# Performance work log

Hardware: AMD Instinct MI355X
Metric: run time of the kernel (lower is better)

Reference implementation:

```python
import jax, jax.numpy as jnp
import numpy as np

B, C, H, D, W = 1, 32, 32, 32, 32   # batch, channels, 3D grid
M1 = M2 = M3 = 16                   # fourier modes kept per dim
KS = 3                              # spatial attention kernel size
MEM = 5                             # memory slots
EPS = 1e-5
N = H * D * W


def _gelu(x):
    return jax.nn.gelu(x, approximate=False)  # torch exact GELU


def _gn(x):
    # GroupNorm(1, C) without affine: normalize over (C,H,D,W) per sample
    mu = jnp.mean(x, axis=(1, 2, 3, 4), keepdims=True)
    var = jnp.var(x, axis=(1, 2, 3, 4), keepdims=True)
    return (x - mu) * jax.lax.rsqrt(var + EPS)


def _spectral_conv(x, wr, wi):
    # classic 3D FNO spectral conv: keep low modes (4 corner blocks in dims H,D; low block in rfft dim W)
    xf = jnp.fft.rfftn(x, axes=(2, 3, 4))                 # (B,C,H,D,W//2+1) complex64
    w = wr + 1j * wi                                      # (4,Cin,Cout,M1,M2,M3)
    of = jnp.zeros((x.shape[0], C, H, D, W // 2 + 1), xf.dtype)
    corners = [(slice(0, M1), slice(0, M2)), (slice(H - M1, H), slice(0, M2)),
               (slice(0, M1), slice(D - M2, D)), (slice(H - M1, H), slice(D - M2, D))]
    for i, (s1, s2) in enumerate(corners):
        of = of.at[:, :, s1, s2, :M3].set(
            jnp.einsum('bixyz,ioxyz->boxyz', xf[:, :, s1, s2, :M3], w[i]))
    return jnp.fft.irfftn(of, s=(H, D, W), axes=(2, 3, 4))


def _forward(x, t, prev_memory, w_spec_r, w_spec_i, norm1_g, norm1_b,
             mlp_w1, mlp_b1, mlp_w2, mlp_b2, tin_gw, tin_gb, tin_bw, tin_bb,
             q_w, q_b, k_w, k_b, v_w, v_b, mem_key, mem_value,
             gate_w, gate_b, gru_wih, gru_whh, gru_bih, gru_bhh):
    skip1 = x
    skip2 = _gelu(x)
    # spectral conv -> GroupNorm(affine) + residual -> gelu
    h = _spectral_conv(x, w_spec_r, w_spec_i)
    h = _gelu(_gn(h) * norm1_g[None, :, None, None, None]
              + norm1_b[None, :, None, None, None] + skip1)
    # pointwise Conv1d MLP over channels
    hf = h.reshape(B, C, N)
    u = _gelu(jnp.einsum('oc,bcn->bon', mlp_w1, hf) + mlp_b1[None, :, None])
    hf = jnp.einsum('oc,bcn->bon', mlp_w2, u) + mlp_b2[None, :, None]
    h = hf.reshape(B, C, H, D, W)
    # time-conditioned instance norm: gamma/beta from 1x1 conv over t (B,C)
    gamma = (jnp.einsum('oc,bc->bo', tin_gw, t) + tin_gb)[:, :, None, None, None]
    beta = (jnp.einsum('oc,bc->bo', tin_bw, t) + tin_bb)[:, :, None, None, None]
    h = gamma * _gn(h) + beta
    # ---- spatial attention with memory ----
    pad = KS // 2
    xp = jnp.pad(h, ((0, 0), (0, 0), (pad, pad), (pad, pad), (pad, pad)))
    # 3D unfold: (B,C,27,N) patches via 27 shifted views
    patches = jnp.stack([xp[:, :, i:i + H, j:j + D, l:l + W]
                         for i in range(KS) for j in range(KS) for l in range(KS)],
                        axis=2).reshape(B, C, KS ** 3, N)
    hf = h.reshape(B, C, N)
    q = jnp.einsum('oc,bcn->bon', q_w, hf) + q_b[None, :, None]              # (B,C,N)
    k_sp = jnp.einsum('oc,bcmn->bomn', k_w, patches) + k_b[None, :, None, None]
    v_sp = jnp.einsum('oc,bcmn->bomn', v_w, patches) + v_b[None, :, None, None]
    mem_k = jnp.broadcast_to(mem_key[None, :, :, None], (B, C, MEM, N))
    mem_v = jnp.broadcast_to(mem_value[None, :, :, None], (B, C, MEM, N))
    k = jnp.concatenate([mem_k, k_sp], axis=2)                               # (B,C,32,N)
    v = jnp.concatenate([mem_v, v_sp], axis=2)
    attn = jax.nn.softmax(q[:, :, None, :] * k / jnp.sqrt(jnp.float32(C)), axis=2)
    out = jnp.sum(attn * v, axis=2)                                          # (B,C,N)
    cat = jnp.concatenate([hf, out], axis=1)                                 # (B,2C,N)
    gate = jax.nn.sigmoid(jnp.einsum('oc,bcn->bon', gate_w, cat) + gate_b[None, :, None])
    out = gate * out + (1.0 - gate) * hf
    out = out.reshape(B, C, H, D, W)
    # GRUCell memory update from spatially pooled features
    m_in = jnp.mean(out, axis=(2, 3, 4))                                     # (B,C)
    gi = m_in @ gru_wih.T + gru_bih
    gh = prev_memory @ gru_whh.T + gru_bhh
    ir, iz, inn = jnp.split(gi, 3, axis=1)
    hr, hz, hn = jnp.split(gh, 3, axis=1)
    r = jax.nn.sigmoid(ir + hr)
    z = jax.nn.sigmoid(iz + hz)
    n = jnp.tanh(inn + r * hn)
    new_memory = (1.0 - z) * n + z * prev_memory                             # (B,C)
    return out + skip2, new_memory


def setup_inputs():
    key = jax.random.key(0)
    ks = jax.random.split(key, 20)
    def rn(k, shape, s):
        return jax.random.normal(k, shape, jnp.float32) * s
    spec_scale = 1.0 / (C * C)
    return dict(
        x=jax.random.normal(ks[0], (B, C, H, D, W), jnp.float32),
        t=jax.random.normal(ks[1], (B, C), jnp.float32),
        prev_memory=jnp.zeros((B, C), jnp.float32),
        w_spec_r=rn(ks[2], (4, C, C, M1, M2, M3), spec_scale),
        w_spec_i=rn(ks[3], (4, C, C, M1, M2, M3), spec_scale),
        norm1_g=jnp.ones((C,), jnp.float32),
        norm1_b=jnp.zeros((C,), jnp.float32),
        mlp_w1=rn(ks[4], (C // 2, C), 0.1), mlp_b1=jnp.zeros((C // 2,), jnp.float32),
        mlp_w2=rn(ks[5], (C, C // 2), 0.1), mlp_b2=jnp.zeros((C,), jnp.float32),
        tin_gw=rn(ks[6], (C, C), 0.1), tin_gb=jnp.ones((C,), jnp.float32),
        tin_bw=rn(ks[7], (C, C), 0.1), tin_bb=jnp.zeros((C,), jnp.float32),
        q_w=rn(ks[8], (C, C), 0.1), q_b=jnp.zeros((C,), jnp.float32),
        k_w=rn(ks[9], (C, C), 0.1), k_b=jnp.zeros((C,), jnp.float32),
        v_w=rn(ks[10], (C, C), 0.1), v_b=jnp.zeros((C,), jnp.float32),
        mem_key=jax.random.normal(ks[11], (C, MEM), jnp.float32),
        mem_value=jax.random.normal(ks[12], (C, MEM), jnp.float32),
        gate_w=rn(ks[13], (C, 2 * C), 0.1), gate_b=jnp.zeros((C,), jnp.float32),
        gru_wih=rn(ks[14], (3 * C, C), 0.1), gru_whh=rn(ks[15], (3 * C, C), 0.1),
        gru_bih=jnp.zeros((3 * C,), jnp.float32), gru_bhh=jnp.zeros((3 * C,), jnp.float32),
    )


def reference(x, t, prev_memory, w_spec_r, w_spec_i, norm1_g, norm1_b,
              mlp_w1, mlp_b1, mlp_w2, mlp_b2, tin_gw, tin_gb, tin_bw, tin_bb,
              q_w, q_b, k_w, k_b, v_w, v_b, mem_key, mem_value,
              gate_w, gate_b, gru_wih, gru_whh, gru_bih, gru_bhh):
    return _forward(x, t, prev_memory, w_spec_r, w_spec_i, norm1_g, norm1_b,
                    mlp_w1, mlp_b1, mlp_w2, mlp_b2, tin_gw, tin_gb, tin_bw, tin_bb,
                    q_w, q_b, k_w, k_b, v_w, v_b, mem_key, mem_value,
                    gate_w, gate_b, gru_wih, gru_whh, gru_bih, gru_bhh)
```

## Files before the change

### kernel.cpp

```cpp
#include <hip/hip_runtime.h>
#include <hip/hip_bf16.h>
#include <math.h>

#define NSP 32768
#define NZ 17

__device__ __forceinline__ float geluf(float x){
    return 0.5f * x * (1.0f + erff(x * 0.70710678118654752f));
}
__device__ __forceinline__ float sigmoidf_(float x){
    return 1.0f / (1.0f + __expf(-x));
}


__global__ void k_fwd(const float* __restrict__ x, float* __restrict__ Br, float* __restrict__ Bi){
    __shared__ float tile[32*33];
    __shared__ float ar[544], ai[544];
    __shared__ float ct[32], st[32];
    int b = blockIdx.x, t = threadIdx.x;
    if (t < 32){ float ang = 6.283185307179586477f * (float)t / 32.0f; ct[t] = cosf(ang); st[t] = sinf(ang); }
    const float* src = x + b * 1024;
    for (int j = t; j < 1024; j += 256) tile[(j & 31) * 33 + (j >> 5)] = src[j];
    __syncthreads();
    for (int idx = t; idx < 544; idx += 256){
        int d = idx / 17, z = idx - d * 17;
        float sr = 0.f, si = 0.f;
        #pragma unroll
        for (int w = 0; w < 32; ++w){
            int a = (z * w) & 31;
            float v = tile[w * 33 + d];
            sr += v * ct[a];
            si -= v * st[a];
        }
        ar[idx] = sr; ai[idx] = si;
    }
    __syncthreads();
    for (int idx = t; idx < 544; idx += 256){
        int kd = idx / 17, z = idx - kd * 17;
        float sr = 0.f, si = 0.f;
        #pragma unroll
        for (int d = 0; d < 32; ++d){
            int a = (kd * d) & 31;
            float c = ct[a], s = st[a];
            float vr = ar[d * 17 + z], vi = ai[d * 17 + z];
            sr += vr * c + vi * s;
            si += vi * c - vr * s;
        }
        Br[b * 544 + idx] = sr; Bi[b * 544 + idx] = si;
    }
}

__global__ void k_fft_h(const float* __restrict__ Br, const float* __restrict__ Bi,
                        float* __restrict__ Ar, float* __restrict__ Ai){
    __shared__ float ir[544], ii[544];
    __shared__ float ct[32], st[32];
    int b = blockIdx.x, t = threadIdx.x;
    int c = b >> 5, d = b & 31;
    if (t < 32){ float ang = 6.283185307179586477f * (float)t / 32.0f; ct[t] = cosf(ang); st[t] = sinf(ang); }
    for (int j = t; j < 544; j += 256){
        int h = j / 17, z = j - h * 17;
        int g = ((c * 32 + h) * 32 + d) * NZ + z;
        ir[j] = Br[g]; ii[j] = Bi[g];
    }
    __syncthreads();
    for (int idx = t; idx < 544; idx += 256){
        int kh = idx / 17, z = idx - kh * 17;
        float sr = 0.f, si = 0.f;
        #pragma unroll
        for (int h = 0; h < 32; ++h){
            int a = (kh * h) & 31;
            float c2 = ct[a], s2 = st[a];
            float vr = ir[h * 17 + z], vi = ii[h * 17 + z];
            sr += vr * c2 + vi * s2;
            si += vi * c2 - vr * s2;
        }
        int g = ((c * 32 + kh) * 32 + d) * NZ + z;
        Ar[g] = sr; Ai[g] = si;
    }
}

__global__ void k_modemul(const float* __restrict__ Xr, const float* __restrict__ Xi,
                          const float* __restrict__ Wr, const float* __restrict__ Wi,
                          float* __restrict__ Or, float* __restrict__ Oi){
    __shared__ float xr[32 * 64], xi[32 * 64];
    int b = blockIdx.x;
    int corner = b >> 6;
    int xm = (b >> 2) & 15;
    int ymg = b & 3;
    int xg = xm + ((corner & 1) << 4);
    int ybase = ymg * 4 + ((corner >> 1) << 4);
    int t = threadIdx.x;
    for (int idx = t; idx < 2048; idx += 1024){
        int i = idx >> 6, m = idx & 63;
        int y = ybase + (m >> 4), z = m & 15;
        int g = ((i * 32 + xg) * 32 + y) * NZ + z;
        xr[idx] = Xr[g]; xi[idx] = Xi[g];
    }
    if (t < 128){
        int o = t >> 2, y = ybase + (t & 3);
        int g = ((o * 32 + xg) * 32 + y) * NZ + 16;
        Or[g] = 0.f; Oi[g] = 0.f;
    }
    __syncthreads();
    int wv = t >> 6, lane = t & 63;
    int o0 = wv * 2, o1 = o0 + 1;
    float ar0 = 0.f, ai0 = 0.f, ar1 = 0.f, ai1 = 0.f;
    int wtail = xm * 256 + ymg * 64 + lane;
    for (int i = 0; i < 32; ++i){
        float vxr = xr[i * 64 + lane], vxi = xi[i * 64 + lane];
        long base = (long)((corner * 32 + i) * 32) * 4096 + wtail;
        float w0r = Wr[base + o0 * 4096], w0i = Wi[base + o0 * 4096];
        float w1r = Wr[base + o1 * 4096], w1i = Wi[base + o1 * 4096];
        ar0 += w0r * vxr - w0i * vxi;
        ai0 += w0r * vxi + w0i * vxr;
        ar1 += w1r * vxr - w1i * vxi;
        ai1 += w1r * vxi + w1i * vxr;
    }
    int y = ybase + (lane >> 4), z = lane & 15;
    int g0 = ((o0 * 32 + xg) * 32 + y) * NZ + z;
    int g1 = ((o1 * 32 + xg) * 32 + y) * NZ + z;
    Or[g0] = ar0; Oi[g0] = ai0;
    Or[g1] = ar1; Oi[g1] = ai1;
}

__global__ void k_ifft_h(const float* __restrict__ Br, const float* __restrict__ Bi,
                         float* __restrict__ Ar, float* __restrict__ Ai){
    __shared__ float ir[544], ii[544];
    __shared__ float ct[32], st[32];
    int b = blockIdx.x, t = threadIdx.x;
    int c = b >> 5, y = b & 31;
    if (t < 32){ float ang = 6.283185307179586477f * (float)t / 32.0f; ct[t] = cosf(ang); st[t] = sinf(ang); }
    for (int j = t; j < 544; j += 256){
        int xk = j / 17, z = j - xk * 17;
        int g = ((c * 32 + xk) * 32 + y) * NZ + z;
        ir[j] = Br[g]; ii[j] = Bi[g];
    }
    __syncthreads();
    for (int idx = t; idx < 544; idx += 256){
        int h = idx / 17, z = idx - h * 17;
        float sr = 0.f, si = 0.f;
        #pragma unroll
        for (int k = 0; k < 32; ++k){
            int a = (k * h) & 31;
            float c2 = ct[a], s2 = st[a];
            float vr = ir[k * 17 + z], vi = ii[k * 17 + z];
            sr += vr * c2 - vi * s2;
            si += vr * s2 + vi * c2;
        }
        int g = ((c * 32 + h) * 32 + y) * NZ + z;
        Ar[g] = sr; Ai[g] = si;
    }
}

__global__ void k_inv(const float* __restrict__ Ar, const float* __restrict__ Ai,
                      float* __restrict__ spec,
                      float* __restrict__ psum, float* __restrict__ psq){
    __shared__ float ir[544], ii[544];
    __shared__ float cr[544], ci[544];
    __shared__ float ct[32], st[32];
    __shared__ float ls[256], lq[256];
    int b = blockIdx.x, t = threadIdx.x;
    if (t < 32){ float ang = 6.283185307179586477f * (float)t / 32.0f; ct[t] = cosf(ang); st[t] = sinf(ang); }
    const float* pr = Ar + b * 544;
    const float* pi = Ai + b * 544;
    for (int j = t; j < 544; j += 256){ ir[j] = pr[j]; ii[j] = pi[j]; }
    __syncthreads();
    for (int idx = t; idx < 544; idx += 256){
        int d = idx / 17, z = idx - d * 17;
        float sr = 0.f, si = 0.f;
        #pragma unroll
        for (int k = 0; k < 32; ++k){
            int a = (k * d) & 31;
            float c2 = ct[a], s2 = st[a];
            float vr = ir[k * 17 + z], vi = ii[k * 17 + z];
            sr += vr * c2 - vi * s2;
            si += vr * s2 + vi * c2;
        }
        cr[idx] = sr; ci[idx] = si;
    }
    __syncthreads();
    const float inv = 1.0f / 32768.0f;
    float s_loc = 0.f, q_loc = 0.f;
    for (int idx = t; idx < 1024; idx += 256){
        int d = idx >> 5, w = idx & 31;
        float s = cr[d * 17 + 0] + ((w & 1) ? -cr[d * 17 + 16] : cr[d * 17 + 16]);
        #pragma unroll
        for (int z = 1; z < 16; ++z){
            int a = (z * w) & 31;
            s += 2.0f * (cr[d * 17 + z] * ct[a] - ci[d * 17 + z] * st[a]);
        }
        s *= inv;
        spec[b * 1024 + idx] = s;
        s_loc += s; q_loc += s * s;
    }
    ls[t] = s_loc; lq[t] = q_loc; __syncthreads();
    for (int off = 128; off > 0; off >>= 1){
        if (t < off){ ls[t] += ls[t + off]; lq[t] += lq[t + off]; }
        __syncthreads();
    }
    if (t == 0){ psum[b] = ls[0]; psq[b] = lq[0]; }
}


__global__ void k_finalize1(const float* __restrict__ psum, const float* __restrict__ psq,
                            int n, float* __restrict__ red){
    __shared__ float ls[256], lq[256];
    int t = threadIdx.x;
    float s = 0.f, q = 0.f;
    for (int j = t; j < n; j += 256){ s += psum[j]; q += psq[j]; }
    ls[t] = s; lq[t] = q; __syncthreads();
    for (int off = 128; off > 0; off >>= 1){
        if (t < off){ ls[t] += ls[t + off]; lq[t] += lq[t + off]; }
        __syncthreads();
    }
    if (t == 0){
        float mu = ls[0] * (1.0f / 1048576.0f);
        float var = lq[0] * (1.0f / 1048576.0f) - mu * mu;
        red[0] = mu; red[1] = rsqrtf(var + 1e-5f);
    }
}

__global__ void k_finalize2(const float* __restrict__ psum, const float* __restrict__ psq,
                            int n, const float* __restrict__ tin,
                            const float* __restrict__ tgw, const float* __restrict__ tgb,
                            const float* __restrict__ tbw, const float* __restrict__ tbb,
                            float* __restrict__ red){
    __shared__ float ls[256], lq[256];
    int t = threadIdx.x;
    float s = 0.f, q = 0.f;
    for (int j = t; j < n; j += 256){ s += psum[j]; q += psq[j]; }
    ls[t] = s; lq[t] = q; __syncthreads();
    for (int off = 128; off > 0; off >>= 1){
        if (t < off){ ls[t] += ls[t + off]; lq[t] += lq[t + off]; }
        __syncthreads();
    }
    if (t == 0){
        float mu = ls[0] * (1.0f / 1048576.0f);
        float var = lq[0] * (1.0f / 1048576.0f) - mu * mu;
        red[2] = mu; red[3] = rsqrtf(var + 1e-5f);
    }
    if (t < 64){
        int o = t & 31;
        const float* w = (t < 32) ? tgw : tbw;
        const float* bi = (t < 32) ? tgb : tbb;
        float a = bi[o];
        #pragma unroll
        for (int c = 0; c < 32; ++c) a += w[o * 32 + c] * tin[c];
        red[(t < 32 ? 16 : 48) + o] = a;
    }
}

__global__ void k_mlp(const float* __restrict__ spec, const float* __restrict__ x,
                      const float* __restrict__ n1g, const float* __restrict__ n1b,
                      const float* __restrict__ red,
                      const float* __restrict__ w1, const float* __restrict__ b1,
                      const float* __restrict__ w2, const float* __restrict__ b2,
                      float* __restrict__ h2,
                      float* __restrict__ psum, float* __restrict__ psq){
    __shared__ float W1[512], W2[512], B1[16], B2[32], GG[32], BB[32];
    __shared__ float ls[256], lq[256];
    int t = threadIdx.x;
    for (int j = t; j < 512; j += 256){ W1[j] = w1[j]; W2[j] = w2[j]; }
    if (t < 16) B1[t] = b1[t];
    if (t < 32){ B2[t] = b2[t]; GG[t] = n1g[t]; BB[t] = n1b[t]; }
    __syncthreads();
    float mu = red[0], rs = red[1];
    int n = blockIdx.x * 256 + t;
    float hv[32];
    #pragma unroll
    for (int c = 0; c < 32; ++c){
        float v = (spec[c * NSP + n] - mu) * rs * GG[c] + BB[c] + x[c * NSP + n];
        hv[c] = geluf(v);
    }
    float u[16];
    #pragma unroll
    for (int o = 0; o < 16; ++o){
        float a = B1[o];
        #pragma unroll
        for (int c = 0; c < 32; ++c) a += W1[o * 32 + c] * hv[c];
        u[o] = geluf(a);
    }
    float s_loc = 0.f, q_loc = 0.f;
    #pragma unroll
    for (int o = 0; o < 32; ++o){
        float a = B2[o];
        #pragma unroll
        for (int c = 0; c < 16; ++c) a += W2[o * 16 + c] * u[c];
        h2[o * NSP + n] = a;
        s_loc += a; q_loc += a * a;
    }
    ls[t] = s_loc; lq[t] = q_loc; __syncthreads();
    for (int off = 128; off > 0; off >>= 1){
        if (t < off){ ls[t] += ls[t + off]; lq[t] += lq[t + off]; }
        __syncthreads();
    }
    if (t == 0){ psum[blockIdx.x] = ls[0]; psq[blockIdx.x] = lq[0]; }
}

__global__ void k_qkv(const float* __restrict__ h2, const float* __restrict__ red,
                      const float* __restrict__ qw, const float* __restrict__ qb,
                      const float* __restrict__ kw, const float* __restrict__ vw,
                      float* __restrict__ h3, float* __restrict__ Q,
                      float* __restrict__ KH, float* __restrict__ VH){
    __shared__ float QW[1024], KW[1024], VW[1024], GA[32], BE[32], QB[32];
    int t = threadIdx.x;
    for (int j = t; j < 1024; j += 256){ QW[j] = qw[j]; KW[j] = kw[j]; VW[j] = vw[j]; }
    if (t < 32){ GA[t] = red[16 + t]; BE[t] = red[48 + t]; QB[t] = qb[t]; }
    __syncthreads();
    float mu = red[2], rs = red[3];
    int n = blockIdx.x * 256 + t;
    float hv[32];
    #pragma unroll
    for (int c = 0; c < 32; ++c){
        float v = GA[c] * ((h2[c * NSP + n] - mu) * rs) + BE[c];
        hv[c] = v;
        h3[c * NSP + n] = v;
    }
    #pragma unroll
    for (int o = 0; o < 32; ++o){
        float aq = QB[o], ak = 0.f, av = 0.f;
        #pragma unroll
        for (int c = 0; c < 32; ++c){
            float v = hv[c];
            aq += QW[o * 32 + c] * v;
            ak += KW[o * 32 + c] * v;
            av += VW[o * 32 + c] * v;
        }
        Q[o * NSP + n] = aq;
        KH[o * NSP + n] = ak;
        VH[o * NSP + n] = av;
    }
}

__global__ void k_attn(const float* __restrict__ Q, const float* __restrict__ KH,
                       const float* __restrict__ VH,
                       const float* __restrict__ kb, const float* __restrict__ vb,
                       const float* __restrict__ mk, const float* __restrict__ mv,
                       float* __restrict__ out0){
    __shared__ float KL[3][1024], VL[3][1024];
    int bid = blockIdx.x;
    int swz = (bid & 7) * 128 + (bid >> 3);
    int c = swz >> 5, h_ = swz & 31;
    int t = threadIdx.x;
    #pragma unroll
    for (int p = 0; p < 3; ++p){
        int hh = h_ - 1 + p;
        if ((unsigned)hh < 32u){
            const float* sk = KH + (c * 32 + hh) * 1024;
            const float* sv = VH + (c * 32 + hh) * 1024;
            for (int j = t; j < 1024; j += 256){ KL[p][j] = sk[j]; VL[p][j] = sv[j]; }
        }
    }
    float kbc = kb[c], vbc = vb[c];
    float mkv[5], mvv[5];
    #pragma unroll
    for (int j = 0; j < 5; ++j){ mkv[j] = mk[c * 5 + j]; mvv[j] = mv[c * 5 + j]; }
    float qv[4];
    #pragma unroll
    for (int i = 0; i < 4; ++i) qv[i] = Q[c * NSP + h_ * 1024 + i * 256 + t];
    __syncthreads();
    const float scale = 0.17677669529663688f;
    #pragma unroll
    for (int i = 0; i < 4; ++i){
        int nl = i * 256 + t;
        int d_ = nl >> 5, w_ = nl & 31;
        float q = qv[i];
        float s = 0.f, acc = 0.f;
        #pragma unroll
        for (int j = 0; j < 5; ++j){
            float e = __expf(q * mkv[j] * scale);
            s += e; acc += e * mvv[j];
        }
        int oob = 0;
        #pragma unroll
        for (int p = 0; p < 3; ++p){
            int hh = h_ - 1 + p;
            if ((unsigned)hh >= 32u){ oob += 9; continue; }
            #pragma unroll
            for (int dj = -1; dj <= 1; ++dj){
                int dd = d_ + dj;
                if ((unsigned)dd >= 32u){ oob += 3; continue; }
                int rb = dd * 32;
                #pragma unroll
                for (int dl = -1; dl <= 1; ++dl){
                    int ww = w_ + dl;
                    if ((unsigned)ww < 32u){
                        float k = kbc + KL[p][rb + ww];
                        float v = vbc + VL[p][rb + ww];
                        float e = __expf(q * k * scale);
                        s += e; acc += e * v;
                    } else oob++;
                }
            }
        }
        float eb = __expf(q * kbc * scale);
        s += (float)oob * eb; acc += (float)oob * eb * vbc;
        out0[c * NSP + h_ * 1024 + nl] = acc / s;
    }
}

__global__ void k_gate(const float* __restrict__ h3, const float* __restrict__ out0,
                       const float* __restrict__ x,
                       const float* __restrict__ gw, const float* __restrict__ gb,
                       float* __restrict__ outp, float* __restrict__ mpart){
    __shared__ float GW[2048];
    __shared__ float FT[32 * 264];
    __shared__ float PS[256];
    int t = threadIdx.x;
    for (int j = t; j < 2048; j += 256) GW[j] = gw[j];
    int n = blockIdx.x * 256 + t;
    float hv[32], ov[32];
    #pragma unroll
    for (int c = 0; c < 32; ++c){ hv[c] = h3[c * NSP + n]; ov[c] = out0[c * NSP + n]; }
    __syncthreads();
    #pragma unroll
    for (int c = 0; c < 32; ++c){
        float g = gb[c];
        #pragma unroll
        for (int cc = 0; cc < 32; ++cc){
            g += GW[c * 64 + cc] * hv[cc] + GW[c * 64 + 32 + cc] * ov[cc];
        }
        g = sigmoidf_(g);
        float fin = g * ov[c] + (1.0f - g) * hv[c];
        FT[c * 264 + t] = fin;
        outp[c * NSP + n] = fin + geluf(x[c * NSP + n]);
    }
    __syncthreads();
    {
        int c8 = t >> 3, seg = t & 7;
        float s = 0.f;
        #pragma unroll
        for (int j = 0; j < 32; ++j) s += FT[c8 * 264 + seg * 32 + j];
        PS[t] = s;
    }
    __syncthreads();
    if (t < 32){
        float s = 0.f;
        #pragma unroll
        for (int j = 0; j < 8; ++j) s += PS[t * 8 + j];
        mpart[t * 128 + blockIdx.x] = s;
    }
}

__global__ void k_mred(const float* __restrict__ mpart, float* __restrict__ red){
    __shared__ float ls[128];
    int c = blockIdx.x, t = threadIdx.x;
    ls[t] = mpart[c * 128 + t];
    __syncthreads();
    for (int off = 64; off > 0; off >>= 1){
        if (t < off) ls[t] += ls[t + off];
        __syncthreads();
    }
    if (t == 0) red[128 + c] = ls[0] * (1.0f / 32768.0f);
}

__global__ void k_gru(const float* __restrict__ red, const float* __restrict__ pm,
                      const float* __restrict__ wih, const float* __restrict__ whh,
                      const float* __restrict__ bih, const float* __restrict__ bhh,
                      float* __restrict__ outp){
    __shared__ float m_in[32], gi[96], gh[96];
    int t = threadIdx.x;
    if (t < 32) m_in[t] = red[128 + t];
    __syncthreads();
    if (t < 96){
        float a = bih[t], b2 = bhh[t];
        #pragma unroll
        for (int cc = 0; cc < 32; ++cc){
            a += wih[t * 32 + cc] * m_in[cc];
            b2 += whh[t * 32 + cc] * pm[cc];
        }
        gi[t] = a; gh[t] = b2;
    }
    __syncthreads();
    if (t < 32){
        float r = sigmoidf_(gi[t] + gh[t]);
        float z = sigmoidf_(gi[32 + t] + gh[32 + t]);
        float nn = tanhf(gi[64 + t] + r * gh[64 + t]);
        float nm = (1.0f - z) * nn + z * pm[t];
        outp[1048576 + t] = nm;
    }
}

extern "C" void kernel_launch(void* const* d_in, const int* in_sizes, int n_in,
                              void* d_out, int out_size, void* d_ws, size_t ws_size,
                              hipStream_t stream){
    const float* x   = (const float*)d_in[0];
    const float* tin = (const float*)d_in[1];
    const float* pm  = (const float*)d_in[2];
    const float* wsr = (const float*)d_in[3];
    const float* wsi = (const float*)d_in[4];
    const float* n1g = (const float*)d_in[5];
    const float* n1b = (const float*)d_in[6];
    const float* mw1 = (const float*)d_in[7];
    const float* mb1 = (const float*)d_in[8];
    const float* mw2 = (const float*)d_in[9];
    const float* mb2 = (const float*)d_in[10];
    const float* tgw = (const float*)d_in[11];
    const float* tgb = (const float*)d_in[12];
    const float* tbw = (const float*)d_in[13];
    const float* tbb = (const float*)d_in[14];
    const float* qw  = (const float*)d_in[15];
    const float* qb  = (const float*)d_in[16];
    const float* kw  = (const float*)d_in[17];
    const float* kb  = (const float*)d_in[18];
    const float* vw  = (const float*)d_in[19];
    const float* vb  = (const float*)d_in[20];
    const float* mk  = (const float*)d_in[21];
    const float* mv  = (const float*)d_in[22];
    const float* gw  = (const float*)d_in[23];
    const float* gb  = (const float*)d_in[24];
    const float* wih = (const float*)d_in[25];
    const float* whh = (const float*)d_in[26];
    const float* bih = (const float*)d_in[27];
    const float* bhh = (const float*)d_in[28];

    float* ws = (float*)d_ws;
    float* Ar   = ws + 0;
    float* Ai   = ws + 557056;
    float* Br   = ws + 1114112;
    float* Bi   = ws + 1671168;
    float* spec = ws + 2228224;
    float* h1   = ws + 3276800;
    float* h2   = ws + 4325376;
    float* h3   = ws + 5373952;
    float* red  = ws + 6422528;
    float* psum = ws + 6422784;
    float* psq  = ws + 6423808;
    float* Qb   = Br;
    float* KHb  = spec;
    float* VHb  = h1;
    float* out0 = Ar;
    float* mpart = h2;

    float* outp = (float*)d_out;

    k_fwd    <<<1024, 256, 0, stream>>>(x, Br, Bi);
    k_fft_h  <<<1024, 256, 0, stream>>>(Br, Bi, Ar, Ai);
    k_modemul<<<256, 1024, 0, stream>>>(Ar, Ai, wsr, wsi, Br, Bi);
    k_ifft_h <<<1024, 256, 0, stream>>>(Br, Bi, Ar, Ai);
    k_inv    <<<1024, 256, 0, stream>>>(Ar, Ai, spec, psum, psq);
    k_finalize1<<<1, 256, 0, stream>>>(psum, psq, 1024, red);
    k_mlp    <<<128, 256, 0, stream>>>(spec, x, n1g, n1b, red, mw1, mb1, mw2, mb2, h2, psum, psq);
    k_finalize2<<<1, 256, 0, stream>>>(psum, psq, 128, tin, tgw, tgb, tbw, tbb, red);
    k_qkv    <<<128, 256, 0, stream>>>(h2, red, qw, qb, kw, vw, h3, Qb, KHb, VHb);
    k_attn   <<<1024, 256, 0, stream>>>(Qb, KHb, VHb, kb, vb, mk, mv, out0);
    k_gate   <<<128, 256, 0, stream>>>(h3, out0, x, gw, gb, outp, mpart);
    k_mred   <<<32, 128, 0, stream>>>(mpart, red);
    k_gru    <<<1, 128, 0, stream>>>(red, pm, wih, whh, bih, bhh, outp);
}
```

Before: 193.7 us.

## Restructure spectral mode multiply with float4 weight loads and larger mode tiles

The mode-multiply kernel is reorganised so each block handles a full 16x16 mode tile for one x-mode and a group of 4 output channels. Each thread now reads four consecutive weights as float4 and computes four modes. The launch changes from 256 blocks of 1024 threads to 512 blocks of 256. This targets the bandwidth-bound streaming of the spectral weights (about 33 MB) by widening loads. In exchange, each block loads a larger input tile into shared memory, and that tile is reloaded by 8 blocks per corner and x-mode.

New measurement: 196.2 us. About the same (+1.3%).

```diff
diff --git a/kernel.cpp b/kernel.cpp
--- a/kernel.cpp
+++ b/kernel.cpp
@@ -82,45 +82,48 @@
 __global__ void k_modemul(const float* __restrict__ Xr, const float* __restrict__ Xi,
                           const float* __restrict__ Wr, const float* __restrict__ Wi,
                           float* __restrict__ Or, float* __restrict__ Oi){
-    __shared__ float xr[32 * 64], xi[32 * 64];
+    __shared__ float xr[32][256], xi[32][256];
     int b = blockIdx.x;
-    int corner = b >> 6;
-    int xm = (b >> 2) & 15;
-    int ymg = b & 3;
+    int corner = b >> 7;
+    int og = (b >> 4) & 7;
+    int xm = b & 15;
     int xg = xm + ((corner & 1) << 4);
-    int ybase = ymg * 4 + ((corner >> 1) << 4);
-    int t = threadIdx.x;
-    for (int idx = t; idx < 2048; idx += 1024){
-        int i = idx >> 6, m = idx & 63;
-        int y = ybase + (m >> 4), z = m & 15;
+    int ybase = (corner >> 1) << 4;
+    int t = threadIdx.x;
+    for (int idx = t; idx < 8192; idx += 256){
+        int i = idx >> 8, mm = idx & 255;
+        int y = ybase + (mm >> 4), z = mm & 15;
         int g = ((i * 32 + xg) * 32 + y) * NZ + z;
-        xr[idx] = Xr[g]; xi[idx] = Xi[g];
-    }
-    if (t < 128){
-        int o = t >> 2, y = ybase + (t & 3);
+        xr[i][mm] = Xr[g]; xi[i][mm] = Xi[g];
+    }
+    if (t < 64){
+        int o = og * 4 + (t >> 4), y = ybase + (t & 15);
         int g = ((o * 32 + xg) * 32 + y) * NZ + 16;
         Or[g] = 0.f; Oi[g] = 0.f;
     }
     __syncthreads();
     int wv = t >> 6, lane = t & 63;
-    int o0 = wv * 2, o1 = o0 + 1;
-    float ar0 = 0.f, ai0 = 0.f, ar1 = 0.f, ai1 = 0.f;
-    int wtail = xm * 256 + ymg * 64 + lane;
+    int o = og * 4 + wv;
+    int m4 = lane * 4;
+    const float* wrbase = Wr + (size_t)((corner * 32) * 32 + o) * 4096 + xm * 256 + m4;
+    const float* wibase = Wi + (size_t)((corner * 32) * 32 + o) * 4096 + xm * 256 + m4;
+    float4 accr = make_float4(0.f, 0.f, 0.f, 0.f);
+    float4 acci = make_float4(0.f, 0.f, 0.f, 0.f);
+    #pragma unroll 8
     for (int i = 0; i < 32; ++i){
-        float vxr = xr[i * 64 + lane], vxi = xi[i * 64 + lane];
-        long base = (long)((corner * 32 + i) * 32) * 4096 + wtail;
-        float w0r = Wr[base + o0 * 4096], w0i = Wi[base + o0 * 4096];
-        float w1r = Wr[base + o1 * 4096], w1i = Wi[base + o1 * 4096];
-        ar0 += w0r * vxr - w0i * vxi;
-        ai0 += w0r * vxi + w0i * vxr;
-        ar1 += w1r * vxr - w1i * vxi;
-        ai1 += w1r * vxi + w1i * vxr;
-    }
-    int y = ybase + (lane >> 4), z = lane & 15;
-    int g0 = ((o0 * 32 + xg) * 32 + y) * NZ + z;
-    int g1 = ((o1 * 32 + xg) * 32 + y) * NZ + z;
-    Or[g0] = ar0; Oi[g0] = ai0;
-    Or[g1] = ar1; Oi[g1] = ai1;
+        float4 w4r = *(const float4*)(wrbase + (size_t)i * 32 * 4096);
+        float4 w4i = *(const float4*)(wibase + (size_t)i * 32 * 4096);
+        float4 x4r = *(const float4*)(&xr[i][m4]);
+        float4 x4i = *(const float4*)(&xi[i][m4]);
+        accr.x += w4r.x * x4r.x - w4i.x * x4i.x;  acci.x += w4r.x * x4i.x + w4i.x * x4r.x;
+        accr.y += w4r.y * x4r.y - w4i.y * x4i.y;  acci.y += w4r.y * x4i.y + w4i.y * x4r.y;
+        accr.z += w4r.z * x4r.z - w4i.z * x4i.z;  acci.z += w4r.z * x4i.z + w4i.z * x4r.z;
+        accr.w += w4r.w * x4r.w - w4i.w * x4i.w;  acci.w += w4r.w * x4i.w + w4i.w * x4r.w;
+    }
+    int y = ybase + (m4 >> 4), zm = m4 & 15;
+    int gb = ((o * 32 + xg) * 32 + y) * NZ + zm;
+    Or[gb + 0] = accr.x; Or[gb + 1] = accr.y; Or[gb + 2] = accr.z; Or[gb + 3] = accr.w;
+    Oi[gb + 0] = acci.x; Oi[gb + 1] = acci.y; Oi[gb + 2] = acci.z; Oi[gb + 3] = acci.w;
 }
 
 __global__ void k_ifft_h(const float* __restrict__ Br, const float* __restrict__ Bi,
@@ -536,7 +539,7 @@
 
     k_fwd    <<<1024, 256, 0, stream>>>(x, Br, Bi);
     k_fft_h  <<<1024, 256, 0, stream>>>(Br, Bi, Ar, Ai);
-    k_modemul<<<256, 1024, 0, stream>>>(Ar, Ai, wsr, wsi, Br, Bi);
+    k_modemul<<<512, 256, 0, stream>>>(Ar, Ai, wsr, wsi, Br, Bi);
     k_ifft_h <<<1024, 256, 0, stream>>>(Br, Bi, Ar, Ai);
     k_inv    <<<1024, 256, 0, stream>>>(Ar, Ai, spec, psum, psq);
     k_finalize1<<<1, 256, 0, stream>>>(psum, psq, 1024, red);
```

## Restructure spectral mode-multiply to one output channel per block with float4 weight loads

Applied to the files above, without the earlier changes.

The mode-multiply kernel now assigns each block one corner, one output channel and a quarter of the modes. Each thread handles four contiguous modes and reads the weights as float4 vectors. The shared-memory staging of inputs is gone; input modes are read straight from global memory, so each input is reloaded by all 32 output channels and relies on cache. The launch changes from 256x1024 to 512x256, and the aim is to stream the large weight tensor more efficiently.

Measured after the change: 191.4 us. About the same (-1.2%).

```diff
diff --git a/kernel.cpp b/kernel.cpp
--- a/kernel.cpp
+++ b/kernel.cpp
@@ -82,45 +82,45 @@
 __global__ void k_modemul(const float* __restrict__ Xr, const float* __restrict__ Xi,
                           const float* __restrict__ Wr, const float* __restrict__ Wi,
                           float* __restrict__ Or, float* __restrict__ Oi){
-    __shared__ float xr[32 * 64], xi[32 * 64];
     int b = blockIdx.x;
-    int corner = b >> 6;
-    int xm = (b >> 2) & 15;
-    int ymg = b & 3;
+    int q = b & 3;
+    int o = (b >> 2) & 31;
+    int corner = b >> 7;
+    int t = threadIdx.x;
+    int m = q * 1024 + t * 4;
+    int xm = m >> 8, ym = (m >> 4) & 15, zm = m & 15;
     int xg = xm + ((corner & 1) << 4);
-    int ybase = ymg * 4 + ((corner >> 1) << 4);
-    int t = threadIdx.x;
-    for (int idx = t; idx < 2048; idx += 1024){
-        int i = idx >> 6, m = idx & 63;
-        int y = ybase + (m >> 4), z = m & 15;
-        int g = ((i * 32 + xg) * 32 + y) * NZ + z;
-        xr[idx] = Xr[g]; xi[idx] = Xi[g];
-    }
+    int y  = ym + ((corner >> 1) << 4);
     if (t < 128){
-        int o = t >> 2, y = ybase + (t & 3);
-        int g = ((o * 32 + xg) * 32 + y) * NZ + 16;
-        Or[g] = 0.f; Oi[g] = 0.f;
-    }
-    __syncthreads();
-    int wv = t >> 6, lane = t & 63;
-    int o0 = wv * 2, o1 = o0 + 1;
-    float ar0 = 0.f, ai0 = 0.f, ar1 = 0.f, ai1 = 0.f;
-    int wtail = xm * 256 + ymg * 64 + lane;
+        int xl = t >> 5;
+        int arr = (t >> 4) & 1;
+        int yl = t & 15;
+        int xgz = q * 4 + xl + ((corner & 1) << 4);
+        int yz = yl + ((corner >> 1) << 4);
+        int g = ((o * 32 + xgz) * 32 + yz) * NZ + 16;
+        if (arr == 0) Or[g] = 0.f; else Oi[g] = 0.f;
+    }
+    size_t xoff = (size_t)(xg * 32 + y) * NZ + zm;
+    const float* wr = Wr + (size_t)((corner * 32) * 32 + o) * 4096 + m;
+    const float* wi = Wi + (size_t)((corner * 32) * 32 + o) * 4096 + m;
+    float ar0=0.f, ar1=0.f, ar2=0.f, ar3=0.f;
+    float ai0=0.f, ai1=0.f, ai2=0.f, ai3=0.f;
+    #pragma unroll 4
     for (int i = 0; i < 32; ++i){
-        float vxr = xr[i * 64 + lane], vxi = xi[i * 64 + lane];
-        long base = (long)((corner * 32 + i) * 32) * 4096 + wtail;
-        float w0r = Wr[base + o0 * 4096], w0i = Wi[base + o0 * 4096];
-        float w1r = Wr[base + o1 * 4096], w1i = Wi[base + o1 * 4096];
-        ar0 += w0r * vxr - w0i * vxi;
-        ai0 += w0r * vxi + w0i * vxr;
-        ar1 += w1r * vxr - w1i * vxi;
-        ai1 += w1r * vxi + w1i * vxr;
-    }
-    int y = ybase + (lane >> 4), z = lane & 15;
-    int g0 = ((o0 * 32 + xg) * 32 + y) * NZ + z;
-    int g1 = ((o1 * 32 + xg) * 32 + y) * NZ + z;
-    Or[g0] = ar0; Oi[g0] = ai0;
-    Or[g1] = ar1; Oi[g1] = ai1;
+        float4 w4r = *(const float4*)(wr + (size_t)i * 131072);
+        float4 w4i = *(const float4*)(wi + (size_t)i * 131072);
+        const float* pxr = Xr + (size_t)i * 17408 + xoff;
+        const float* pxi = Xi + (size_t)i * 17408 + xoff;
+        float xr0 = pxr[0], xr1 = pxr[1], xr2 = pxr[2], xr3 = pxr[3];
+        float xi0 = pxi[0], xi1 = pxi[1], xi2 = pxi[2], xi3 = pxi[3];
+        ar0 += w4r.x * xr0 - w4i.x * xi0;  ai0 += w4r.x * xi0 + w4i.x * xr0;
+        ar1 += w4r.y * xr1 - w4i.y * xi1;  ai1 += w4r.y * xi1 + w4i.y * xr1;
+        ar2 += w4r.z * xr2 - w4i.z * xi2;  ai2 += w4r.z * xi2 + w4i.z * xr2;
+        ar3 += w4r.w * xr3 - w4i.w * xi3;  ai3 += w4r.w * xi3 + w4i.w * xr3;
+    }
+    int g = ((o * 32 + xg) * 32 + y) * NZ + zm;
+    Or[g + 0] = ar0; Or[g + 1] = ar1; Or[g + 2] = ar2; Or[g + 3] = ar3;
+    Oi[g + 0] = ai0; Oi[g + 1] = ai1; Oi[g + 2] = ai2; Oi[g + 3] = ai3;
 }
 
 __global__ void k_ifft_h(const float* __restrict__ Br, const float* __restrict__ Bi,
@@ -536,7 +536,7 @@
 
     k_fwd    <<<1024, 256, 0, stream>>>(x, Br, Bi);
     k_fft_h  <<<1024, 256, 0, stream>>>(Br, Bi, Ar, Ai);
-    k_modemul<<<256, 1024, 0, stream>>>(Ar, Ai, wsr, wsi, Br, Bi);
+    k_modemul<<<512, 256, 0, stream>>>(Ar, Ai, wsr, wsi, Br, Bi);
     k_ifft_h <<<1024, 256, 0, stream>>>(Br, Bi, Ar, Ai);
     k_inv    <<<1024, 256, 0, stream>>>(Ar, Ai, spec, psum, psq);
     k_finalize1<<<1, 256, 0, stream>>>(psum, psq, 1024, red);
```
